# Kernel tuning notes

Hardware: AMD Instinct MI355X
Metric: run time of the kernel (lower is better)

The kernel has to match this reference:

```python
import jax, jax.numpy as jnp
import numpy as np

B, C, H, W, L = 8, 512, 32, 32, 10
CQK = C // 8
EPS = 1e-5


def conv1x1(x, Wt, b):
    # 1x1 conv == per-pixel linear: [O,C] x [B,C,H,W] -> [B,O,H,W]
    return jnp.einsum('oc,bchw->bohw', Wt, x) + b[None, :, None, None]


def batchnorm_train(x, g, b):
    # BatchNorm2d in training mode: batch stats over (N,H,W), biased variance
    m = x.mean(axis=(0, 2, 3))
    v = x.var(axis=(0, 2, 3))
    inv = jax.lax.rsqrt(v + EPS)
    return (x - m[None, :, None, None]) * (g * inv)[None, :, None, None] + b[None, :, None, None]


def setup_inputs() -> dict:
    key = jax.random.key(0)
    ks = jax.random.split(key, 24)
    s = lambda n: 1.0 / np.sqrt(n)
    inp = {
        'x': jax.random.normal(ks[0], (B, C, H, W), jnp.float32),
        'y': jax.random.normal(ks[1], (B, C, H, W), jnp.float32),
        'x_hidden': jax.random.normal(ks[2], (L, B, C, H, W), jnp.float32),
        'y_hidden': jax.random.normal(ks[3], (L, B, C, H, W), jnp.float32),
        'qW': jax.random.normal(ks[4], (CQK, C), jnp.float32) * s(C),
        'qb': jnp.zeros((CQK,), jnp.float32),
        'kW': jax.random.normal(ks[5], (CQK, C), jnp.float32) * s(C),
        'kb': jnp.zeros((CQK,), jnp.float32),
        'v1W': jax.random.normal(ks[6], (C, C), jnp.float32) * s(C),
        'v1b': jnp.zeros((C,), jnp.float32),
        'v2W': jax.random.normal(ks[7], (C, C), jnp.float32) * s(C),
        'v2b': jnp.zeros((C,), jnp.float32),
        'hw1': jnp.ones((L,), jnp.float32),
        'hw2': jnp.ones((L,), jnp.float32),
        'g1W1': jax.random.normal(ks[8], (64, C), jnp.float32) * s(C),
        'g1b1': jnp.zeros((64,), jnp.float32),
        'g1W2': jax.random.normal(ks[9], (1, 64), jnp.float32) * s(64),
        'g1b2': jnp.zeros((1,), jnp.float32),
        'g2W1': jax.random.normal(ks[10], (64, C), jnp.float32) * s(C),
        'g2b1': jnp.zeros((64,), jnp.float32),
        'g2W2': jax.random.normal(ks[11], (1, 64), jnp.float32) * s(64),
        'g2b2': jnp.zeros((1,), jnp.float32),
        'rW1': jax.random.normal(ks[12], (C, C), jnp.float32) * s(C),
        'rb1': jnp.zeros((C,), jnp.float32),
        'bn1g': jnp.ones((C,), jnp.float32),
        'bn1b': jnp.zeros((C,), jnp.float32),
        'rW2': jax.random.normal(ks[13], (C, C), jnp.float32) * s(C),
        'rb2': jnp.zeros((C,), jnp.float32),
        'bn2g': jnp.ones((C,), jnp.float32),
        'bn2b': jnp.zeros((C,), jnp.float32),
    }
    return inp


def reference(x, y, x_hidden, y_hidden, qW, qb, kW, kb, v1W, v1b, v2W, v2b,
              hw1, hw2, g1W1, g1b1, g1W2, g1b2, g2W1, g2b1, g2W2, g2b2,
              rW1, rb1, bn1g, bn1b, rW2, rb2, bn2g, bn2b):
    b_, c_, h_, w_ = x.shape
    n = h_ * w_

    def residual(z):
        z1 = jax.nn.relu(batchnorm_train(conv1x1(z, rW1, rb1), bn1g, bn1b))
        return batchnorm_train(conv1x1(z1, rW2, rb2), bn2g, bn2b)

    # QKV projections (1x1 convs), flattened to tokens
    q = conv1x1(x, qW, qb).reshape(b_, CQK, n).transpose(0, 2, 1)   # [B,N,Cqk]
    k = conv1x1(y, kW, kb).reshape(b_, CQK, n)                       # [B,Cqk,N]
    v1 = conv1x1(x, v1W, v1b).reshape(b_, c_, n)                     # [B,C,N]
    v2 = conv1x1(y, v2W, v2b).reshape(b_, c_, n)

    attn = jax.nn.softmax(jnp.einsum('bnd,bdm->bnm', q, k), axis=-1)  # [B,N,N]
    out1 = jnp.einsum('bcn,bmn->bcm', v1, attn).reshape(b_, c_, h_, w_)  # v1 @ attn^T
    out2 = jnp.einsum('bcn,bnm->bcm', v2, attn).reshape(b_, c_, h_, w_)  # v2 @ attn

    # hidden-layer weighted channel means -> gamma scalars
    num_layers = min(x_hidden.shape[0], L)
    xw = jax.nn.softmax(hw1[:num_layers])
    yw = jax.nn.softmax(hw2[:num_layers])
    x_hw = jnp.einsum('l,lbc->bc', xw, x_hidden[:num_layers].mean(axis=(3, 4)))  # [B,C]
    y_hw = jnp.einsum('l,lbc->bc', yw, y_hidden[:num_layers].mean(axis=(3, 4)))

    def gamma_gen(v, W1, b1, W2, b2):
        h1 = jax.nn.relu(v @ W1.T + b1)
        return (h1 @ W2.T + b2).reshape(b_, 1, 1, 1)

    gamma1 = gamma_gen(x_hw, g1W1, g1b1, g1W2, g1b2)
    gamma2 = gamma_gen(y_hw, g2W1, g2b1, g2W2, g2b2)

    out1 = jax.nn.relu(residual(gamma1 * out1) + x)
    out2 = jax.nn.relu(residual(gamma2 * out2) + y)
    return out1, out2
```

## Files before the change

kernel.cpp:

```cpp
#include <hip/hip_runtime.h>

#define BB 8
#define CC 512
#define NT 1024
#define LL 10
#define DQK 64
#define BN_EPS 1e-5f

using u16 = unsigned short;
typedef __attribute__((ext_vector_type(8))) short short8;
typedef __attribute__((ext_vector_type(4))) float f32x4;
typedef __attribute__((ext_vector_type(4))) float nf4;

__device__ __forceinline__ float waveSum(float v) {
#pragma unroll
  for (int o = 32; o; o >>= 1) v += __shfl_down(v, o, 64);
  return v;
}
__device__ __forceinline__ float waveMax(float v) {
#pragma unroll
  for (int o = 32; o; o >>= 1) v = fmaxf(v, __shfl_down(v, o, 64));
  return v;
}
__device__ __forceinline__ u16 f2bf(float f) {
  unsigned u = __float_as_uint(f);
  u += 0x7FFFu + ((u >> 16) & 1u);
  return (u16)(u >> 16);
}
__device__ __forceinline__ float bf2f(u16 h) {
  return __uint_as_float(((unsigned)h) << 16);
}
__device__ __forceinline__ void g2l16(const u16* g, void* l) {
  __builtin_amdgcn_global_load_lds(
      (const __attribute__((address_space(1))) unsigned int*)g,
      (__attribute__((address_space(3))) unsigned int*)l, 16, 0, 0);
}

__device__ __forceinline__ void hidden_mean_block(
    int mb, const float* __restrict__ xh, const float* __restrict__ yh,
    float* __restrict__ lm) {
  int wid = mb * 4 + ((int)threadIdx.x >> 6);
  int lane = threadIdx.x & 63;
  const int LBC = LL * BB * CC;
  const float* src = xh;
  int r = wid;
  if (wid >= LBC) { src = yh; r = wid - LBC; }
  const nf4* p = (const nf4*)(src + (size_t)r * NT);
  nf4 v0 = __builtin_nontemporal_load(p + lane);
  nf4 v1 = __builtin_nontemporal_load(p + 64 + lane);
  nf4 v2 = __builtin_nontemporal_load(p + 128 + lane);
  nf4 v3 = __builtin_nontemporal_load(p + 192 + lane);
  float s = ((v0.x + v0.y) + (v0.z + v0.w)) + ((v1.x + v1.y) + (v1.z + v1.w)) +
            ((v2.x + v2.y) + (v2.z + v2.w)) + ((v3.x + v3.y) + (v3.z + v3.w));
  s = waveSum(s);
  if (lane == 0) lm[wid] = s * (1.0f / NT);
}

struct PreArgs {
  const float *v1W, *v2W, *rW1, *rW2;
  u16* Wdst;
  const float *qW, *kW;
  u16 *qh, *ql, *kh, *kl;
  const float *qb, *kb, *v1b, *v2b;
  float *qkb, *vb;
  const float *x, *y;
  u16 *xth, *xtl, *yth, *ytl;
};
__global__ __launch_bounds__(256) void pre_kernel(PreArgs a) {
  __shared__ float t[64][65];
  const int blk = blockIdx.x;
  if (blk < 1024) {
    int rel = blk;
    const float* srcs[4] = {a.v1W, a.v2W, a.rW1, a.rW2};
    const float4* s4 = (const float4*)srcs[rel >> 8];
    int r = rel & 255;
    float4 v = s4[(size_t)r * 256 + threadIdx.x];
    uint2 o;
    o.x = (unsigned)f2bf(v.x) | ((unsigned)f2bf(v.y) << 16);
    o.y = (unsigned)f2bf(v.z) | ((unsigned)f2bf(v.w) << 16);
    ((uint2*)a.Wdst)[(size_t)rel * 256 + threadIdx.x] = o;
  } else if (blk < 1088) {
    int rel = blk - 1024;
    if (rel == 0) {
      int tt = threadIdx.x;
      if (tt < 64) a.qkb[tt] = a.qb[tt];
      else if (tt < 128) a.qkb[tt] = a.kb[tt - 64];
      a.vb[tt] = a.v1b[tt]; a.vb[tt + 256] = a.v1b[tt + 256];
      a.vb[tt + 512] = a.v2b[tt]; a.vb[tt + 768] = a.v2b[tt + 256];
    }
    const float* src = (rel < 32) ? a.qW : a.kW;
    u16* dh = (rel < 32) ? a.qh : a.kh;
    u16* dl = (rel < 32) ? a.ql : a.kl;
    int r = rel & 31;
    float4 v = ((const float4*)src)[(size_t)r * 256 + threadIdx.x];
    u16 h0 = f2bf(v.x), h1 = f2bf(v.y), h2 = f2bf(v.z), h3 = f2bf(v.w);
    u16 l0 = f2bf(v.x - bf2f(h0)), l1 = f2bf(v.y - bf2f(h1));
    u16 l2 = f2bf(v.z - bf2f(h2)), l3 = f2bf(v.w - bf2f(h3));
    uint2 oh, ol;
    oh.x = (unsigned)h0 | ((unsigned)h1 << 16); oh.y = (unsigned)h2 | ((unsigned)h3 << 16);
    ol.x = (unsigned)l0 | ((unsigned)l1 << 16); ol.y = (unsigned)l2 | ((unsigned)l3 << 16);
    ((uint2*)dh)[(size_t)r * 256 + threadIdx.x] = oh;
    ((uint2*)dl)[(size_t)r * 256 + threadIdx.x] = ol;
  } else {
    int rel = blk - 1088;
    int z = rel >> 7;
    const float* src = (z < 8) ? a.x : a.y;
    u16* dh = (z < 8) ? a.xth : a.yth;
    u16* dl = (z < 8) ? a.xtl : a.ytl;
    int b = z & 7;
    int n0 = (rel & 15) * 64, c0 = ((rel >> 4) & 7) * 64;
    int tc = threadIdx.x & 63, tr = threadIdx.x >> 6;
    const float* S = src + ((size_t)b * CC + c0) * NT + n0;
#pragma unroll
    for (int r = 0; r < 16; r++) {
      int c = tr + r * 4;
      t[c][tc] = S[(size_t)c * NT + tc];
    }
    __syncthreads();
    size_t base = ((size_t)b * NT + n0) * CC + c0;
#pragma unroll
    for (int r = 0; r < 16; r++) {
      int n = tr + r * 4;
      float v = t[tc][n];
      u16 h = f2bf(v);
      dh[base + (size_t)n * CC + tc] = h;
      dl[base + (size_t)n * CC + tc] = f2bf(v - bf2f(h));
    }
  }
}

__global__ __launch_bounds__(256) void gamma_kernel(
    const float* __restrict__ lm,
    const float* __restrict__ hw1, const float* __restrict__ hw2,
    const float* __restrict__ g1W1, const float* __restrict__ g1b1,
    const float* __restrict__ g1W2, const float* __restrict__ g1b2,
    const float* __restrict__ g2W1, const float* __restrict__ g2b1,
    const float* __restrict__ g2W2, const float* __restrict__ g2b2,
    float* __restrict__ gamma) {
  int which = blockIdx.x >> 3;
  int b = blockIdx.x & 7;
  const float* hw = which ? hw2 : hw1;
  const float* W1 = which ? g2W1 : g1W1;
  const float* b1 = which ? g2b1 : g1b1;
  const float* W2 = which ? g2W2 : g1W2;
  const float* b2 = which ? g2b2 : g1b2;
  __shared__ float sxhw[CC];
  __shared__ float wsm[LL];
  if (threadIdx.x == 0) {
    float mx = -1e30f;
    for (int l = 0; l < LL; l++) mx = fmaxf(mx, hw[l]);
    float den = 0.f, e[LL];
    for (int l = 0; l < LL; l++) { e[l] = __expf(hw[l] - mx); den += e[l]; }
    for (int l = 0; l < LL; l++) wsm[l] = e[l] / den;
  }
  __syncthreads();
  const float* lmb = lm + (size_t)which * LL * BB * CC + b * CC;
  for (int c = threadIdx.x; c < CC; c += blockDim.x) {
    float a = 0.f;
    for (int l = 0; l < LL; l++) a += wsm[l] * lmb[l * BB * CC + c];
    sxhw[c] = a;
  }
  __syncthreads();
  float contrib = 0.f;
  if (threadIdx.x < 64) {
    int d = threadIdx.x;
    float a = b1[d];
    const float* wr = W1 + d * CC;
    for (int c = 0; c < CC; c++) a = fmaf(wr[c], sxhw[c], a);
    contrib = W2[d] * fmaxf(a, 0.f);
  }
  contrib = waveSum(contrib);
  if (threadIdx.x == 0) gamma[which * BB + b] = contrib + b2[0];
}

__global__ __launch_bounds__(256) void transpose_attn_kernel(
    const u16* __restrict__ attn, u16* __restrict__ attnT) {
  __shared__ u16 t[64][66];
  int b = blockIdx.z;
  int n0 = blockIdx.y * 64, m0 = blockIdx.x * 64;
  int tc = threadIdx.x & 63, tr = threadIdx.x >> 6;
  const u16* S = attn + ((size_t)b * NT + n0) * NT + m0;
#pragma unroll
  for (int r = 0; r < 16; r++) {
    int nr = tr + r * 4;
    t[nr][tc] = S[(size_t)nr * NT + tc];
  }
  __syncthreads();
  u16* D = attnT + ((size_t)b * NT + m0) * NT + n0;
#pragma unroll
  for (int r = 0; r < 16; r++) {
    int mr = tr + r * 4;
    D[(size_t)mr * NT + tc] = t[tc][mr];
  }
}

template <int BN, int SMODE, int GMODE>
__global__ __launch_bounds__(256) void gemm_bf16(
    const u16* __restrict__ A, long long sA, int lda,
    const u16* __restrict__ B, long long sB, long long sB2, int ldb,
    void* __restrict__ C, long long sC, int ldc,
    int K, int storef32,
    const float* __restrict__ bias_row, int brs,
    const float* __restrict__ scale,
    float* __restrict__ pS, float* __restrict__ pS2,
    int xbits, int ybits, int nReal,
    int meanBase, const float* __restrict__ xh, const float* __restrict__ yh,
    float* __restrict__ lm) {
  constexpr int BM = 128, BK = 32;
  constexpr int WN = (BN == 128) ? 2 : 1;
  constexpr int WM = 4 / WN;
  constexpr int FM = BM / (WM * 16);
  constexpr int FN = BN / (WN * 16);
  __shared__ u16 As[BM * BK];
  __shared__ u16 Bs[BN * BK];
  int bx, by, bz;
  if (nReal > 0) {
    int id = blockIdx.x;
    if (id >= nReal) { hidden_mean_block(meanBase + (id - nReal), xh, yh, lm); return; }
    bx = id & ((1 << xbits) - 1);
    by = (id >> xbits) & ((1 << ybits) - 1);
    bz = id >> (xbits + ybits);
  } else {
    bx = blockIdx.x; by = blockIdx.y; bz = blockIdx.z;
  }
  const int i0 = by * BM;
  const int j0 = bx * BN;
  const u16* Ab = A + (size_t)bz * sA + (size_t)i0 * lda;
  const u16* Bb = B + (size_t)(bz & 7) * sB + (size_t)(bz >> 3) * sB2 + (size_t)j0 * ldb;
  const int tid = threadIdx.x;
  const int lane = tid & 63;
  const int wave = tid >> 6;
  const int wr = wave / WN, wc = wave % WN;
  const int fr = lane & 15;
  const int kg = lane >> 4;
  const int arow = tid >> 2;
  const int aq = tid & 3;

  f32x4 acc[FM][FN] = {};

  for (int k0 = 0; k0 < K; k0 += BK) {
#pragma unroll
    for (int c = 0; c < (BM * BK * 2) / 4096; c++)
      g2l16(Ab + (size_t)(arow + c * 64) * lda + k0 + aq * 8,
            (char*)As + c * 4096 + tid * 16);
#pragma unroll
    for (int c = 0; c < (BN * BK * 2) / 4096; c++)
      g2l16(Bb + (size_t)(arow + c * 64) * ldb + k0 + aq * 8,
            (char*)Bs + c * 4096 + tid * 16);
    __syncthreads();
    short8 fa[FM], fb[FN];
#pragma unroll
    for (int i = 0; i < FM; i++)
      fa[i] = *(const short8*)&As[(wr * FM * 16 + i * 16 + fr) * BK + kg * 8];
#pragma unroll
    for (int j = 0; j < FN; j++)
      fb[j] = *(const short8*)&Bs[(wc * FN * 16 + j * 16 + fr) * BK + kg * 8];
#pragma unroll
    for (int i = 0; i < FM; i++)
#pragma unroll
      for (int j = 0; j < FN; j++)
        acc[i][j] = __builtin_amdgcn_mfma_f32_16x16x32_bf16(fa[i], fb[j], acc[i][j], 0, 0, 0);
    __syncthreads();
  }

  const float scl = (GMODE == 0 && scale) ? scale[bz] : 1.0f;
  const float* brow = bias_row ? bias_row + (size_t)bz * brs : nullptr;
  float* Cf = (float*)C + (size_t)bz * sC;
  u16* Ch = (u16*)C + (size_t)bz * sC;
  float cs[FN] = {}, cs2[FN] = {};
  float rs[FM * 4] = {}, rs2[FM * 4] = {};
#pragma unroll
  for (int i = 0; i < FM; i++) {
#pragma unroll
    for (int j = 0; j < FN; j++) {
      int col = j0 + wc * FN * 16 + j * 16 + fr;
#pragma unroll
      for (int r = 0; r < 4; r++) {
        int row = i0 + wr * FM * 16 + i * 16 + kg * 4 + r;
        float rb = brow ? brow[row] : 0.0f;
        float sc2 = scl;
        if constexpr (GMODE == 1) sc2 = scale[((row >> 13) << 3) + ((row >> 10) & 7)];
        float v = (acc[i][j][r] + rb) * sc2;
        if constexpr (SMODE == 1) { cs[j] += v; cs2[j] += v * v; }
        if constexpr (SMODE == 2) { rs[i * 4 + r] += v; rs2[i * 4 + r] += v * v; }
        if (storef32) Cf[(size_t)row * ldc + col] = v;
        else Ch[(size_t)row * ldc + col] = f2bf(v);
      }
    }
  }

  if constexpr (SMODE == 1) {
    __shared__ float sred[2][4][FN][16];
#pragma unroll
    for (int j = 0; j < FN; j++) {
      float s = cs[j], s2 = cs2[j];
      s += __shfl_xor(s, 16, 64); s += __shfl_xor(s, 32, 64);
      s2 += __shfl_xor(s2, 16, 64); s2 += __shfl_xor(s2, 32, 64);
      if (lane < 16) { sred[0][wr][j][lane] = s; sred[1][wr][j][lane] = s2; }
    }
    __syncthreads();
    if (tid < FN * 16) {
      int j = tid >> 4, f = tid & 15;
      float s = sred[0][0][j][f] + sred[0][1][j][f] + sred[0][2][j][f] + sred[0][3][j][f];
      float s2 = sred[1][0][j][f] + sred[1][1][j][f] + sred[1][2][j][f] + sred[1][3][j][f];
      int col = j0 + j * 16 + f;
      int chain = by >> 6, ib = by & 63;
      pS[((size_t)chain * 512 + col) * 64 + ib] = s;
      pS2[((size_t)chain * 512 + col) * 64 + ib] = s2;
    }
  }
  if constexpr (SMODE == 2) {
#pragma unroll
    for (int i = 0; i < FM; i++)
#pragma unroll
      for (int r = 0; r < 4; r++) {
        float s = rs[i * 4 + r], s2 = rs2[i * 4 + r];
        s += __shfl_xor(s, 1, 64); s += __shfl_xor(s, 2, 64);
        s += __shfl_xor(s, 4, 64); s += __shfl_xor(s, 8, 64);
        s2 += __shfl_xor(s2, 1, 64); s2 += __shfl_xor(s2, 2, 64);
        s2 += __shfl_xor(s2, 4, 64); s2 += __shfl_xor(s2, 8, 64);
        if (fr == 0) {
          int row = i0 + wr * FM * 16 + i * 16 + kg * 4 + r;
          pS[((size_t)bz * 512 + row) * 128 + bx] = s;
          pS2[((size_t)bz * 512 + row) * 128 + bx] = s2;
        }
      }
  }
}

__global__ __launch_bounds__(256) void gemm_split(
    const u16* __restrict__ Ah_, const u16* __restrict__ Al_, long long sA, int lda,
    const u16* __restrict__ Bh_, const u16* __restrict__ Bl_, long long sB, int ldb,
    float* __restrict__ Cf, u16* __restrict__ Ch, u16* __restrict__ Cl,
    long long sC, int ldc, int K, const float* __restrict__ bias_col, int bcs,
    int xbits, int ybits, int nReal,
    int meanBase, const float* __restrict__ xh, const float* __restrict__ yh,
    float* __restrict__ lm) {
  constexpr int BM = 128, BN = 64, BK = 32;
  constexpr int FM = 2, FN = 4;
  __shared__ u16 Ahs[BM * BK];
  __shared__ u16 Als[BM * BK];
  __shared__ u16 Bhs[BN * BK];
  __shared__ u16 Bls[BN * BK];
  int bx, by, bz;
  {
    int id = blockIdx.x;
    if (id >= nReal) { hidden_mean_block(meanBase + (id - nReal), xh, yh, lm); return; }
    bx = id & ((1 << xbits) - 1);
    by = (id >> xbits) & ((1 << ybits) - 1);
    bz = id >> (xbits + ybits);
  }
  const int i0 = by * BM;
  const int j0 = bx * BN;
  const u16* Abh = Ah_ + (size_t)bz * sA + (size_t)i0 * lda;
  const u16* Abl = Al_ + (size_t)bz * sA + (size_t)i0 * lda;
  const u16* Bbh = Bh_ + (size_t)bz * sB + (size_t)j0 * ldb;
  const u16* Bbl = Bl_ + (size_t)bz * sB + (size_t)j0 * ldb;
  const int tid = threadIdx.x;
  const int lane = tid & 63;
  const int wr = tid >> 6;
  const int fr = lane & 15;
  const int kg = lane >> 4;
  const int arow = tid >> 2;
  const int aq = tid & 3;

  f32x4 acc[FM][FN] = {};

  for (int k0 = 0; k0 < K; k0 += BK) {
#pragma unroll
    for (int c = 0; c < 2; c++) {
      g2l16(Abh + (size_t)(arow + c * 64) * lda + k0 + aq * 8,
            (char*)Ahs + c * 4096 + tid * 16);
      g2l16(Abl + (size_t)(arow + c * 64) * lda + k0 + aq * 8,
            (char*)Als + c * 4096 + tid * 16);
    }
    g2l16(Bbh + (size_t)arow * ldb + k0 + aq * 8, (char*)Bhs + tid * 16);
    g2l16(Bbl + (size_t)arow * ldb + k0 + aq * 8, (char*)Bls + tid * 16);
    __syncthreads();
    short8 fah[FM], fal[FM], fbh[FN], fbl[FN];
#pragma unroll
    for (int i = 0; i < FM; i++) {
      fah[i] = *(const short8*)&Ahs[(wr * 32 + i * 16 + fr) * BK + kg * 8];
      fal[i] = *(const short8*)&Als[(wr * 32 + i * 16 + fr) * BK + kg * 8];
    }
#pragma unroll
    for (int j = 0; j < FN; j++) {
      fbh[j] = *(const short8*)&Bhs[(j * 16 + fr) * BK + kg * 8];
      fbl[j] = *(const short8*)&Bls[(j * 16 + fr) * BK + kg * 8];
    }
#pragma unroll
    for (int i = 0; i < FM; i++)
#pragma unroll
      for (int j = 0; j < FN; j++) {
        acc[i][j] = __builtin_amdgcn_mfma_f32_16x16x32_bf16(fah[i], fbh[j], acc[i][j], 0, 0, 0);
        acc[i][j] = __builtin_amdgcn_mfma_f32_16x16x32_bf16(fah[i], fbl[j], acc[i][j], 0, 0, 0);
        acc[i][j] = __builtin_amdgcn_mfma_f32_16x16x32_bf16(fal[i], fbh[j], acc[i][j], 0, 0, 0);
      }
    __syncthreads();
  }

  const float* bcol = bias_col ? bias_col + (size_t)bz * bcs : nullptr;
  float* Cfb = Cf ? Cf + (size_t)bz * sC : nullptr;
  u16* Chb = Ch ? Ch + (size_t)bz * sC : nullptr;
  u16* Clb = Cl ? Cl + (size_t)bz * sC : nullptr;
#pragma unroll
  for (int i = 0; i < FM; i++) {
#pragma unroll
    for (int j = 0; j < FN; j++) {
      int col = j0 + j * 16 + fr;
      float cb = bcol ? bcol[col] : 0.0f;
#pragma unroll
      for (int r = 0; r < 4; r++) {
        int row = i0 + wr * 32 + i * 16 + kg * 4 + r;
        float v = acc[i][j][r] + cb;
        if (Cfb) {
          Cfb[(size_t)row * ldc + col] = v;
        } else {
          u16 h = f2bf(v);
          Chb[(size_t)row * ldc + col] = h;
          Clb[(size_t)row * ldc + col] = f2bf(v - bf2f(h));
        }
      }
    }
  }
}

__global__ __launch_bounds__(256) void softmax_bf_kernel(
    const float* __restrict__ S, u16* __restrict__ A) {
  const float4* row = (const float4*)(S + (size_t)blockIdx.x * NT);
  float4 v = row[threadIdx.x];
  __shared__ float sb[4];
  __shared__ float broad;
  int lane = threadIdx.x & 63, wid = threadIdx.x >> 6;
  float mx = fmaxf(fmaxf(v.x, v.y), fmaxf(v.z, v.w));
  mx = waveMax(mx);
  if (lane == 0) sb[wid] = mx;
  __syncthreads();
  if (threadIdx.x == 0) broad = fmaxf(fmaxf(sb[0], sb[1]), fmaxf(sb[2], sb[3]));
  __syncthreads();
  mx = broad;
  v.x = __expf(v.x - mx); v.y = __expf(v.y - mx);
  v.z = __expf(v.z - mx); v.w = __expf(v.w - mx);
  float s = v.x + v.y + v.z + v.w;
  s = waveSum(s);
  __syncthreads();
  if (lane == 0) sb[wid] = s;
  __syncthreads();
  if (threadIdx.x == 0) broad = sb[0] + sb[1] + sb[2] + sb[3];
  __syncthreads();
  float inv = 1.0f / broad;
  uint2 o;
  o.x = (unsigned)f2bf(v.x * inv) | ((unsigned)f2bf(v.y * inv) << 16);
  o.y = (unsigned)f2bf(v.z * inv) | ((unsigned)f2bf(v.w * inv) << 16);
  ((uint2*)(A + (size_t)blockIdx.x * NT))[threadIdx.x] = o;
}

template <int NP>
__global__ __launch_bounds__(128) void bnstats_reduce_np(
    const float* __restrict__ pS, const float* __restrict__ pS2,
    const float* __restrict__ g, const float* __restrict__ bet,
    float* __restrict__ scale, float* __restrict__ shift) {
  int cg = blockIdx.x;
  int c = cg & 511;
  int t = threadIdx.x;
  float s = 0.f, s2 = 0.f;
  if (t < NP) { s = pS[(size_t)cg * NP + t]; s2 = pS2[(size_t)cg * NP + t]; }
  s = waveSum(s); s2 = waveSum(s2);
  __shared__ float sb[4];
  int lane = t & 63, wid = t >> 6;
  if (lane == 0) { sb[wid] = s; sb[wid + 2] = s2; }
  __syncthreads();
  if (t == 0) {
    float S = sb[0] + sb[1];
    float S2 = sb[2] + sb[3];
    const float invn = 1.0f / (BB * NT);
    float mean = S * invn;
    float var = S2 * invn - mean * mean;
    float inv = rsqrtf(var + BN_EPS);
    float sc = g[c] * inv;
    scale[cg] = sc;
    shift[cg] = bet[c] - mean * sc;
  }
}

__global__ __launch_bounds__(256) void bn_apply_kernel(
    const u16* __restrict__ Z, u16* __restrict__ Zo,
    const float* __restrict__ scale, const float* __restrict__ shift) {
  size_t e4 = (size_t)blockIdx.x * 256 + threadIdx.x;
  int chain = (int)(e4 >> 20);
  int c = (int)(e4 & 127) * 4 + chain * 512;
  uint2 u = ((const uint2*)Z)[e4];
  float a = bf2f((u16)u.x), b = bf2f((u16)(u.x >> 16));
  float d = bf2f((u16)u.y), e = bf2f((u16)(u.y >> 16));
  a = fmaxf(fmaf(a, scale[c], shift[c]), 0.f);
  b = fmaxf(fmaf(b, scale[c + 1], shift[c + 1]), 0.f);
  d = fmaxf(fmaf(d, scale[c + 2], shift[c + 2]), 0.f);
  e = fmaxf(fmaf(e, scale[c + 3], shift[c + 3]), 0.f);
  uint2 o;
  o.x = (unsigned)f2bf(a) | ((unsigned)f2bf(b) << 16);
  o.y = (unsigned)f2bf(d) | ((unsigned)f2bf(e) << 16);
  ((uint2*)Zo)[e4] = o;
}

__global__ __launch_bounds__(256) void bn_final_kernel(
    const u16* __restrict__ Z2, const float* __restrict__ X, const float* __restrict__ Y,
    const float* __restrict__ scale, const float* __restrict__ shift,
    float* __restrict__ Out) {
  size_t e = (size_t)blockIdx.x * 256 + threadIdx.x;
  int chain = (int)(e >> 20);
  size_t ec = e & 1048575;
  int c = (int)(ec >> 11);
  int r = (int)(ec & 2047);
  int b = r >> 8;
  uint2 u = ((const uint2*)Z2)[e];
  float a0 = bf2f((u16)u.x), a1 = bf2f((u16)(u.x >> 16));
  float a2 = bf2f((u16)u.y), a3 = bf2f((u16)(u.y >> 16));
  float sc = scale[c + chain * 512], sh = shift[c + chain * 512];
  size_t xi = ((size_t)b * CC + c) * 256 + (r & 255);
  const float* Xs = chain ? Y : X;
  float4 xv = ((const float4*)Xs)[xi];
  float4 o;
  o.x = fmaxf(fmaf(a0, sc, sh) + xv.x, 0.f);
  o.y = fmaxf(fmaf(a1, sc, sh) + xv.y, 0.f);
  o.z = fmaxf(fmaf(a2, sc, sh) + xv.z, 0.f);
  o.w = fmaxf(fmaf(a3, sc, sh) + xv.w, 0.f);
  ((float4*)(Out + (size_t)chain * 4194304))[xi] = o;
}

extern "C" void kernel_launch(void* const* d_in, const int* in_sizes, int n_in,
                              void* d_out, int out_size, void* d_ws, size_t ws_size,
                              hipStream_t stream) {
  (void)in_sizes; (void)n_in; (void)out_size; (void)ws_size;
  const float* x    = (const float*)d_in[0];
  const float* y    = (const float*)d_in[1];
  const float* xh   = (const float*)d_in[2];
  const float* yh   = (const float*)d_in[3];
  const float* qW   = (const float*)d_in[4];
  const float* qb   = (const float*)d_in[5];
  const float* kW   = (const float*)d_in[6];
  const float* kb   = (const float*)d_in[7];
  const float* v1W  = (const float*)d_in[8];
  const float* v1b  = (const float*)d_in[9];
  const float* v2W  = (const float*)d_in[10];
  const float* v2b  = (const float*)d_in[11];
  const float* hw1  = (const float*)d_in[12];
  const float* hw2  = (const float*)d_in[13];
  const float* g1W1 = (const float*)d_in[14];
  const float* g1b1 = (const float*)d_in[15];
  const float* g1W2 = (const float*)d_in[16];
  const float* g1b2 = (const float*)d_in[17];
  const float* g2W1 = (const float*)d_in[18];
  const float* g2b1 = (const float*)d_in[19];
  const float* g2W2 = (const float*)d_in[20];
  const float* g2b2 = (const float*)d_in[21];
  const float* rW1  = (const float*)d_in[22];
  const float* bn1g = (const float*)d_in[24];
  const float* bn1b = (const float*)d_in[25];
  const float* rW2  = (const float*)d_in[26];
  const float* bn2g = (const float*)d_in[28];
  const float* bn2b = (const float*)d_in[29];
  float* out = (float*)d_out;

  float* ws  = (float*)d_ws;
  float* lm  = ws;
  float* gam = ws + 81920;
  float* scA = ws + 81936;
  float* shA = ws + 82960;
  float* qkb = ws + 83984;
  float* vb  = ws + 84112;
  float* pS  = ws + 85136;
  float* pS2 = ws + 347280;
  float* S   = ws + 609424;
  u16* U     = (u16*)(ws + 8998032);
  u16* Wqh = U;
  u16* Wql = U + 32768;
  u16* Wkh = U + 65536;
  u16* Wkl = U + 98304;
  u16* Wv1 = U + 131072;
  u16* Wv2 = U + 393216;
  u16* Wr1 = U + 655360;
  u16* Wr2 = U + 917504;
  u16* xth = U + 1179648;
  u16* yth = xth + 4194304;
  u16* xtl = yth + 4194304;
  u16* ytl = xtl + 4194304;
  u16* q_h = ytl + 4194304;
  u16* q_l = q_h + 524288;
  u16* k_h = q_l + 524288;
  u16* k_l = k_h + 524288;
  u16* v1  = k_l + 524288;
  u16* v2  = v1 + 4194304;
  u16* attn  = v2 + 4194304;
  u16* attnT = attn + 8388608;
  u16* o1t = xth;
  u16* z0  = v1;
  u16* z1  = xth;
  u16* z2  = attn;

  PreArgs pa;
  pa.v1W = v1W; pa.v2W = v2W; pa.rW1 = rW1; pa.rW2 = rW2; pa.Wdst = Wv1;
  pa.qW = qW; pa.kW = kW; pa.qh = Wqh; pa.ql = Wql; pa.kh = Wkh; pa.kl = Wkl;
  pa.qb = qb; pa.kb = kb; pa.v1b = v1b; pa.v2b = v2b; pa.qkb = qkb; pa.vb = vb;
  pa.x = x; pa.y = y; pa.xth = xth; pa.xtl = xtl; pa.yth = yth; pa.ytl = ytl;
  pre_kernel<<<3136, 256, 0, stream>>>(pa);

  gemm_bf16<128, 0, 0><<<512 + 5120, 256, 0, stream>>>(
      Wv1, 262144, CC, xth, 4194304, 0, CC, v1, 4194304, BB * NT, CC, 0, vb, 512,
      nullptr, nullptr, nullptr, 6, 2, 512, 0, xh, yh, lm);
  gemm_split<<<128 + 3072, 256, 0, stream>>>(
      xth, xtl, 4194304, CC, Wqh, Wql, 65536, CC,
      nullptr, q_h, q_l, 1048576, DQK, CC, qkb, 64,
      0, 6, 128, 5120, xh, yh, lm);

  gemm_split<<<1024 + 4096, 256, 0, stream>>>(
      q_h, q_l, (long long)NT * DQK, DQK, k_h, k_l, (long long)NT * DQK, DQK,
      S, nullptr, nullptr, (long long)NT * NT, NT, DQK, nullptr, 0,
      4, 3, 1024, 8192, xh, yh, lm);
  softmax_bf_kernel<<<BB * NT, 256, 0, stream>>>(S, attn);
  transpose_attn_kernel<<<dim3(16, 16, 8), 256, 0, stream>>>(attn, attnT);

  gemm_bf16<128, 0, 0><<<512 + 8192, 256, 0, stream>>>(
      attn, (long long)NT * NT, NT, v1, NT, 4194304, BB * NT,
      o1t, (long long)NT * CC, CC, NT, 0, nullptr, 0, nullptr, nullptr, nullptr,
      2, 3, 512, 12288, xh, yh, lm);

  gamma_kernel<<<16, 256, 0, stream>>>(lm, hw1, hw2, g1W1, g1b1, g1W2, g1b2,
                                       g2W1, g2b1, g2W2, g2b2, gam);
  gemm_bf16<64, 1, 1><<<dim3(8, 128, 1), 256, 0, stream>>>(
      o1t, 0, CC, Wr1, 0, 0, CC, z0, 0, CC, CC, 0, nullptr, 0, gam, pS, pS2,
      0, 0, 0, 0, nullptr, nullptr, nullptr);
  bnstats_reduce_np<64><<<1024, 128, 0, stream>>>(pS, pS2, bn1g, bn1b, scA, shA);
  bn_apply_kernel<<<8192, 256, 0, stream>>>(z0, z1, scA, shA);
  gemm_bf16<64, 2, 0><<<dim3(128, 4, 2), 256, 0, stream>>>(
      Wr2, 0, CC, z1, 4194304, 0, CC, z2, 4194304, BB * NT, CC, 0, nullptr, 0, nullptr,
      pS, pS2, 0, 0, 0, 0, nullptr, nullptr, nullptr);
  bnstats_reduce_np<128><<<1024, 128, 0, stream>>>(pS, pS2, bn2g, bn2b, scA, shA);
  bn_final_kernel<<<8192, 256, 0, stream>>>(z2, x, y, scA, shA, out);
}
```

Measured before the change: 268.5 us.

## Fuse softmax exponentiation into QK GEMM epilogue with deferred row normalization

The QK^T split GEMM now applies exp(s - 20) in its epilogue and writes the unnormalized bf16 probabilities directly. It also writes per-tile partial row sums. This removes the fp32 score matrix round-trip and the separate softmax kernel. A small kernel turns the partial sums into inverse row sums. The transpose kernel applies them, and the attn·V GEMM applies them as a per-row epilogue scale. In exchange, a fixed shift replaces the per-row max, which can overflow if scores exceed roughly 100, and row sums are taken over bf16-rounded values.

```diff
diff --git a/kernel.cpp b/kernel.cpp
--- a/kernel.cpp
+++ b/kernel.cpp
@@ -15,11 +15,6 @@
 __device__ __forceinline__ float waveSum(float v) {
 #pragma unroll
   for (int o = 32; o; o >>= 1) v += __shfl_down(v, o, 64);
-  return v;
-}
-__device__ __forceinline__ float waveMax(float v) {
-#pragma unroll
-  for (int o = 32; o; o >>= 1) v = fmaxf(v, __shfl_down(v, o, 64));
   return v;
 }
 __device__ __forceinline__ u16 f2bf(float f) {
@@ -173,8 +168,19 @@
   if (threadIdx.x == 0) gamma[which * BB + b] = contrib + b2[0];
 }
 
+__global__ __launch_bounds__(256) void rowsum_inv_kernel(
+    const float* __restrict__ pRS, float* __restrict__ rsinv) {
+  int r = blockIdx.x * 256 + threadIdx.x;
+  const float4* p = (const float4*)(pRS + (size_t)r * 16);
+  float4 a = p[0], b = p[1], c = p[2], d = p[3];
+  float s = ((a.x + a.y) + (a.z + a.w)) + ((b.x + b.y) + (b.z + b.w)) +
+            ((c.x + c.y) + (c.z + c.w)) + ((d.x + d.y) + (d.z + d.w));
+  rsinv[r] = 1.0f / s;
+}
+
 __global__ __launch_bounds__(256) void transpose_attn_kernel(
-    const u16* __restrict__ attn, u16* __restrict__ attnT) {
+    const u16* __restrict__ attn, u16* __restrict__ attnT,
+    const float* __restrict__ rsinv) {
   __shared__ u16 t[64][66];
   int b = blockIdx.z;
   int n0 = blockIdx.y * 64, m0 = blockIdx.x * 64;
@@ -187,10 +193,11 @@
   }
   __syncthreads();
   u16* D = attnT + ((size_t)b * NT + m0) * NT + n0;
+  float ri = rsinv[(size_t)b * NT + n0 + tc];
 #pragma unroll
   for (int r = 0; r < 16; r++) {
     int mr = tr + r * 4;
-    D[(size_t)mr * NT + tc] = t[tc][mr];
+    D[(size_t)mr * NT + tc] = f2bf(bf2f(t[tc][mr]) * ri);
   }
 }
 
@@ -280,6 +287,7 @@
         float rb = brow ? brow[row] : 0.0f;
         float sc2 = scl;
         if constexpr (GMODE == 1) sc2 = scale[((row >> 13) << 3) + ((row >> 10) & 7)];
+        if constexpr (GMODE == 2) sc2 = (bz < 8) ? scale[(size_t)bz * NT + row] : 1.0f;
         float v = (acc[i][j][r] + rb) * sc2;
         if constexpr (SMODE == 1) { cs[j] += v; cs2[j] += v * v; }
         if constexpr (SMODE == 2) { rs[i * 4 + r] += v; rs2[i * 4 + r] += v * v; }
@@ -328,11 +336,13 @@
   }
 }
 
+template <int EMODE>
 __global__ __launch_bounds__(256) void gemm_split(
     const u16* __restrict__ Ah_, const u16* __restrict__ Al_, long long sA, int lda,
     const u16* __restrict__ Bh_, const u16* __restrict__ Bl_, long long sB, int ldb,
     float* __restrict__ Cf, u16* __restrict__ Ch, u16* __restrict__ Cl,
     long long sC, int ldc, int K, const float* __restrict__ bias_col, int bcs,
+    float* __restrict__ pRS,
     int xbits, int ybits, int nReal,
     int meanBase, const float* __restrict__ xh, const float* __restrict__ yh,
     float* __restrict__ lm) {
@@ -399,60 +409,62 @@
     __syncthreads();
   }
 
-  const float* bcol = bias_col ? bias_col + (size_t)bz * bcs : nullptr;
-  float* Cfb = Cf ? Cf + (size_t)bz * sC : nullptr;
-  u16* Chb = Ch ? Ch + (size_t)bz * sC : nullptr;
-  u16* Clb = Cl ? Cl + (size_t)bz * sC : nullptr;
-#pragma unroll
-  for (int i = 0; i < FM; i++) {
-#pragma unroll
-    for (int j = 0; j < FN; j++) {
-      int col = j0 + j * 16 + fr;
-      float cb = bcol ? bcol[col] : 0.0f;
-#pragma unroll
-      for (int r = 0; r < 4; r++) {
-        int row = i0 + wr * 32 + i * 16 + kg * 4 + r;
-        float v = acc[i][j][r] + cb;
-        if (Cfb) {
-          Cfb[(size_t)row * ldc + col] = v;
-        } else {
-          u16 h = f2bf(v);
+  if constexpr (EMODE == 1) {
+    u16* Chb = Ch + (size_t)bz * sC;
+    float rsum[FM * 4] = {};
+#pragma unroll
+    for (int i = 0; i < FM; i++) {
+#pragma unroll
+      for (int j = 0; j < FN; j++) {
+        int col = j0 + j * 16 + fr;
+#pragma unroll
+        for (int r = 0; r < 4; r++) {
+          int row = i0 + wr * 32 + i * 16 + kg * 4 + r;
+          float p = __expf(acc[i][j][r] - 20.0f);
+          u16 h = f2bf(p);
           Chb[(size_t)row * ldc + col] = h;
-          Clb[(size_t)row * ldc + col] = f2bf(v - bf2f(h));
+          rsum[i * 4 + r] += bf2f(h);
         }
       }
     }
-  }
-}
-
-__global__ __launch_bounds__(256) void softmax_bf_kernel(
-    const float* __restrict__ S, u16* __restrict__ A) {
-  const float4* row = (const float4*)(S + (size_t)blockIdx.x * NT);
-  float4 v = row[threadIdx.x];
-  __shared__ float sb[4];
-  __shared__ float broad;
-  int lane = threadIdx.x & 63, wid = threadIdx.x >> 6;
-  float mx = fmaxf(fmaxf(v.x, v.y), fmaxf(v.z, v.w));
-  mx = waveMax(mx);
-  if (lane == 0) sb[wid] = mx;
-  __syncthreads();
-  if (threadIdx.x == 0) broad = fmaxf(fmaxf(sb[0], sb[1]), fmaxf(sb[2], sb[3]));
-  __syncthreads();
-  mx = broad;
-  v.x = __expf(v.x - mx); v.y = __expf(v.y - mx);
-  v.z = __expf(v.z - mx); v.w = __expf(v.w - mx);
-  float s = v.x + v.y + v.z + v.w;
-  s = waveSum(s);
-  __syncthreads();
-  if (lane == 0) sb[wid] = s;
-  __syncthreads();
-  if (threadIdx.x == 0) broad = sb[0] + sb[1] + sb[2] + sb[3];
-  __syncthreads();
-  float inv = 1.0f / broad;
-  uint2 o;
-  o.x = (unsigned)f2bf(v.x * inv) | ((unsigned)f2bf(v.y * inv) << 16);
-  o.y = (unsigned)f2bf(v.z * inv) | ((unsigned)f2bf(v.w * inv) << 16);
-  ((uint2*)(A + (size_t)blockIdx.x * NT))[threadIdx.x] = o;
+#pragma unroll
+    for (int i = 0; i < FM; i++)
+#pragma unroll
+      for (int r = 0; r < 4; r++) {
+        float s = rsum[i * 4 + r];
+        s += __shfl_xor(s, 1, 64); s += __shfl_xor(s, 2, 64);
+        s += __shfl_xor(s, 4, 64); s += __shfl_xor(s, 8, 64);
+        if (fr == 0) {
+          int row = i0 + wr * 32 + i * 16 + kg * 4 + r;
+          pRS[((size_t)bz * NT + row) * 16 + bx] = s;
+        }
+      }
+  } else {
+    const float* bcol = bias_col ? bias_col + (size_t)bz * bcs : nullptr;
+    float* Cfb = Cf ? Cf + (size_t)bz * sC : nullptr;
+    u16* Chb = Ch ? Ch + (size_t)bz * sC : nullptr;
+    u16* Clb = Cl ? Cl + (size_t)bz * sC : nullptr;
+#pragma unroll
+    for (int i = 0; i < FM; i++) {
+#pragma unroll
+      for (int j = 0; j < FN; j++) {
+        int col = j0 + j * 16 + fr;
+        float cb = bcol ? bcol[col] : 0.0f;
+#pragma unroll
+        for (int r = 0; r < 4; r++) {
+          int row = i0 + wr * 32 + i * 16 + kg * 4 + r;
+          float v = acc[i][j][r] + cb;
+          if (Cfb) {
+            Cfb[(size_t)row * ldc + col] = v;
+          } else {
+            u16 h = f2bf(v);
+            Chb[(size_t)row * ldc + col] = h;
+            Clb[(size_t)row * ldc + col] = f2bf(v - bf2f(h));
+          }
+        }
+      }
+    }
+  }
 }
 
 template <int NP>
@@ -570,7 +582,8 @@
   float* vb  = ws + 84112;
   float* pS  = ws + 85136;
   float* pS2 = ws + 347280;
-  float* S   = ws + 609424;
+  float* pRS = ws + 609424;
+  float* rsv = ws + 740496;
   u16* U     = (u16*)(ws + 8998032);
   u16* Wqh = U;
   u16* Wql = U + 32768;
@@ -607,21 +620,21 @@
   gemm_bf16<128, 0, 0><<<512 + 5120, 256, 0, stream>>>(
       Wv1, 262144, CC, xth, 4194304, 0, CC, v1, 4194304, BB * NT, CC, 0, vb, 512,
       nullptr, nullptr, nullptr, 6, 2, 512, 0, xh, yh, lm);
-  gemm_split<<<128 + 3072, 256, 0, stream>>>(
+  gemm_split<0><<<128 + 3072, 256, 0, stream>>>(
       xth, xtl, 4194304, CC, Wqh, Wql, 65536, CC,
-      nullptr, q_h, q_l, 1048576, DQK, CC, qkb, 64,
+      nullptr, q_h, q_l, 1048576, DQK, CC, qkb, 64, nullptr,
       0, 6, 128, 5120, xh, yh, lm);
 
-  gemm_split<<<1024 + 4096, 256, 0, stream>>>(
+  gemm_split<1><<<1024 + 4096, 256, 0, stream>>>(
       q_h, q_l, (long long)NT * DQK, DQK, k_h, k_l, (long long)NT * DQK, DQK,
-      S, nullptr, nullptr, (long long)NT * NT, NT, DQK, nullptr, 0,
+      nullptr, attn, nullptr, (long long)NT * NT, NT, DQK, nullptr, 0, pRS,
       4, 3, 1024, 8192, xh, yh, lm);
-  softmax_bf_kernel<<<BB * NT, 256, 0, stream>>>(S, attn);
-  transpose_attn_kernel<<<dim3(16, 16, 8), 256, 0, stream>>>(attn, attnT);
-
-  gemm_bf16<128, 0, 0><<<512 + 8192, 256, 0, stream>>>(
+  rowsum_inv_kernel<<<32, 256, 0, stream>>>(pRS, rsv);
+  transpose_attn_kernel<<<dim3(16, 16, 8), 256, 0, stream>>>(attn, attnT, rsv);
+
+  gemm_bf16<128, 0, 2><<<512 + 8192, 256, 0, stream>>>(
       attn, (long long)NT * NT, NT, v1, NT, 4194304, BB * NT,
-      o1t, (long long)NT * CC, CC, NT, 0, nullptr, 0, nullptr, nullptr, nullptr,
+      o1t, (long long)NT * CC, CC, NT, 0, nullptr, 0, rsv, nullptr, nullptr,
       2, 3, 512, 12288, xh, yh, lm);
 
   gamma_kernel<<<16, 256, 0, stream>>>(lm, hw1, hw2, g1W1, g1b1, g1W2, g1b2,
```

Result: no change. 263.6 us (-1.8%).
